# Kernel tuning notes

Hardware: AMD Instinct MI355X
Metric: run time of the kernel (lower is better)

## Reference

```python
import jax, jax.numpy as jnp
import numpy as np

H = 16  # n_heads


def setup_inputs() -> dict:
    key = jax.random.key(0)
    ks = jax.random.split(key, 11)
    B, S, D = 2, 2048, 1024
    def rn(k, shape, scale=1.0):
        return jax.random.normal(k, shape, dtype=jnp.float32) * scale
    w_scale = 1.0 / np.sqrt(D)
    return {
        "queries": rn(ks[0], (B, S, D)),
        "keys": rn(ks[1], (B, S, D)),
        "values": rn(ks[2], (B, S, D)),
        "Wq": rn(ks[3], (D, D), w_scale), "bq": rn(ks[4], (D,), 0.02),
        "Wk": rn(ks[5], (D, D), w_scale), "bk": rn(ks[6], (D,), 0.02),
        "Wv": rn(ks[7], (D, D), w_scale), "bv": rn(ks[8], (D,), 0.02),
        "Wo": rn(ks[9], (D, D), w_scale), "bo": rn(ks[10], (D,), 0.02),
    }


def _split_heads(x, h):
    # [B, S, D] -> [B, h, S, D/h]
    B, S, D = x.shape
    return x.reshape(B, S, h, D // h).transpose(0, 2, 1, 3)


def reference(queries, keys, values, Wq, bq, Wk, bk, Wv, bv, Wo, bo):
    B, S, D = queries.shape
    Q = _split_heads(queries @ Wq + bq, H)  # [B,h,S,dk]
    K = _split_heads(keys @ Wk + bk, H)
    V = _split_heads(values @ Wv + bv, H)
    # Faithful quirk: scale by sqrt(seq_len), not sqrt(d_k)
    factor = jnp.sqrt(jnp.asarray(S, dtype=Q.dtype))
    scores = jnp.einsum("bhqd,bhkd->bhqk", Q, K) / factor  # [B,h,S,S]
    weights = jax.nn.softmax(scores, axis=-1)
    attn = jnp.einsum("bhqk,bhkd->bhqd", weights, V)  # [B,h,S,dk]
    attn = attn.transpose(0, 2, 1, 3).reshape(B, S, D)  # [B,S,D]
    return attn @ Wo + bo
```

## Files before the change

### kernel.cpp

```cpp
#include <hip/hip_runtime.h>

typedef unsigned short ushort_t;
typedef unsigned int uint_t;
typedef __attribute__((ext_vector_type(8))) short short8;
typedef __attribute__((ext_vector_type(4))) float floatx4;

#define QSCALE 0.03187936f

__device__ __forceinline__ ushort_t f2bf(float f) {
    union { float f; uint_t u; } c; c.f = f;
    uint_t u = c.u;
    return (ushort_t)((u + 0x7fffu + ((u >> 16) & 1u)) >> 16);
}
__device__ __forceinline__ floatx4 mfma16x32(short8 a, short8 b, floatx4 c) {
    return __builtin_amdgcn_mfma_f32_16x16x32_bf16(a, b, c, 0, 0, 0);
}
__device__ __forceinline__ floatx4 zero4() { floatx4 z = {0.f, 0.f, 0.f, 0.f}; return z; }

__device__ __forceinline__ void gload16(const ushort_t* g, ushort_t* l) {
    __builtin_amdgcn_global_load_lds(
        (const __attribute__((address_space(1))) void*)g,
        (__attribute__((address_space(3))) void*)l, 16, 0, 0);
}

__global__ __launch_bounds__(256) void cvt_bf16(
    const float* __restrict__ s0, const float* __restrict__ s1,
    const float* __restrict__ s2, ushort_t* __restrict__ d0,
    ushort_t* __restrict__ d1, ushort_t* __restrict__ d2)
{
    const int which = blockIdx.x >> 11;
    const int blk = blockIdx.x & 2047;
    const float* src = (which == 0) ? s0 : (which == 1) ? s1 : s2;
    ushort_t* dst = (which == 0) ? d0 : (which == 1) ? d1 : d2;
    const int i = (blk * 256 + threadIdx.x) * 8;
    float4 f0 = *(const float4*)(src + i);
    float4 f1 = *(const float4*)(src + i + 4);
    __align__(16) ushort_t t[8];
    t[0] = f2bf(f0.x); t[1] = f2bf(f0.y); t[2] = f2bf(f0.z); t[3] = f2bf(f0.w);
    t[4] = f2bf(f1.x); t[5] = f2bf(f1.y); t[6] = f2bf(f1.z); t[7] = f2bf(f1.w);
    *(uint4*)(dst + i) = *(uint4*)t;
}

__global__ __launch_bounds__(256) void transpose_w(
    const float* __restrict__ W0, const float* __restrict__ W1,
    const float* __restrict__ W2, const float* __restrict__ W3,
    ushort_t* __restrict__ WT)
{
    __shared__ ushort_t tile[64][65];
    const float* W = (blockIdx.y == 0) ? W0 : (blockIdx.y == 1) ? W1
                   : (blockIdx.y == 2) ? W2 : W3;
    ushort_t* dst = WT + (size_t)blockIdx.y * (1024 * 1024);
    const int t = threadIdx.x;
    const int r = t >> 2, p = t & 3;
    const int j0 = (blockIdx.x & 15) << 6, k0 = (blockIdx.x >> 4) << 6;

    const float* src = W + (size_t)(k0 + r) * 1024 + j0 + p * 16;
    float4 f0 = *(const float4*)(src);
    float4 f1 = *(const float4*)(src + 4);
    float4 f2 = *(const float4*)(src + 8);
    float4 f3 = *(const float4*)(src + 12);
    ushort_t* tr = &tile[r][p * 16];
    tr[0] = f2bf(f0.x); tr[1] = f2bf(f0.y); tr[2]  = f2bf(f0.z); tr[3]  = f2bf(f0.w);
    tr[4] = f2bf(f1.x); tr[5] = f2bf(f1.y); tr[6]  = f2bf(f1.z); tr[7]  = f2bf(f1.w);
    tr[8] = f2bf(f2.x); tr[9] = f2bf(f2.y); tr[10] = f2bf(f2.z); tr[11] = f2bf(f2.w);
    tr[12] = f2bf(f3.x); tr[13] = f2bf(f3.y); tr[14] = f2bf(f3.z); tr[15] = f2bf(f3.w);
    __syncthreads();
    __align__(16) ushort_t buf[16];
#pragma unroll
    for (int i = 0; i < 16; ++i) buf[i] = tile[p * 16 + i][r];
    ushort_t* o = dst + (size_t)(j0 + r) * 1024 + k0 + p * 16;
    *(uint4*)(o)     = *(uint4*)(buf);
    *(uint4*)(o + 8) = *(uint4*)(buf + 8);
}

__global__ __launch_bounds__(256) void gemm_bt(
    const ushort_t* __restrict__ A0, const ushort_t* __restrict__ A1,
    const ushort_t* __restrict__ A2, const ushort_t* __restrict__ WT,
    const float* __restrict__ b0, const float* __restrict__ b1,
    const float* __restrict__ b2,
    ushort_t* __restrict__ Dq, ushort_t* __restrict__ Dk,
    ushort_t* __restrict__ Dv, int zbase)
{
    __shared__ __align__(16) ushort_t As[128 * 32];
    __shared__ __align__(16) ushort_t Bs[128 * 32];

    const int mode = blockIdx.z + zbase;
    const ushort_t* A = (mode == 0) ? A0 : (mode == 1) ? A1 : A2;
    const float* bias = (mode == 0) ? b0 : (mode == 1) ? b1 : b2;
    const ushort_t* Bt = WT + (size_t)mode * 1048576;

    const int tid = threadIdx.x;
    const int lane = tid & 63, wid = tid >> 6;
    const int quad = lane >> 4, l16 = lane & 15;
    const int wm = wid >> 1, wn = wid & 1;
    const int row0 = blockIdx.y << 7, col0 = blockIdx.x << 7;

    floatx4 acc[4][4];
#pragma unroll
    for (int i = 0; i < 4; ++i)
#pragma unroll
        for (int j = 0; j < 4; ++j) acc[i][j] = zero4();

    const int i0 = tid, i1 = 256 + tid;
    const int r0_ = i0 >> 2, c0_ = (i0 & 3) ^ (r0_ & 3);
    const int r1_ = i1 >> 2, c1_ = (i1 & 3) ^ (r1_ & 3);
    const ushort_t* gA0 = A  + (size_t)(row0 + r0_) * 1024 + c0_ * 8;
    const ushort_t* gA1 = A  + (size_t)(row0 + r1_) * 1024 + c1_ * 8;
    const ushort_t* gB0 = Bt + (size_t)(col0 + r0_) * 1024 + c0_ * 8;
    const ushort_t* gB1 = Bt + (size_t)(col0 + r1_) * 1024 + c1_ * 8;
    ushort_t* lA0 = As + i0 * 8;  ushort_t* lA1 = As + i1 * 8;
    ushort_t* lB0 = Bs + i0 * 8;  ushort_t* lB1 = Bs + i1 * 8;

    const int ra = wm * 64 + l16, rb = wn * 64 + l16;
    const int sa_off = (quad ^ (l16 & 3)) * 8;

    for (int k0 = 0; k0 < 1024; k0 += 32) {
        __syncthreads();
        gload16(gA0 + k0, lA0);
        gload16(gA1 + k0, lA1);
        gload16(gB0 + k0, lB0);
        gload16(gB1 + k0, lB1);
        __syncthreads();

        short8 af[4], bf[4];
#pragma unroll
        for (int i = 0; i < 4; ++i)
            af[i] = *(const short8*)(As + (ra + i * 16) * 32 + sa_off);
#pragma unroll
        for (int j = 0; j < 4; ++j)
            bf[j] = *(const short8*)(Bs + (rb + j * 16) * 32 + sa_off);
#pragma unroll
        for (int i = 0; i < 4; ++i)
#pragma unroll
            for (int j = 0; j < 4; ++j)
                acc[i][j] = mfma16x32(af[i], bf[j], acc[i][j]);
    }

    const float sc = (mode == 0) ? QSCALE : 1.f;
#pragma unroll
    for (int i = 0; i < 4; ++i) {
#pragma unroll
        for (int j = 0; j < 4; ++j) {
            const int c = col0 + wn * 64 + j * 16 + l16;
            const float bv = bias[c];
#pragma unroll
            for (int rr = 0; rr < 4; ++rr) {
                const int r = row0 + wm * 64 + i * 16 + quad * 4 + rr;
                const float v = (acc[i][j][rr] + bv) * sc;
                const int b = r >> 11, s = r & 2047, h = c >> 6, d = c & 63;
                if (mode <= 1) {
                    ushort_t* D = (mode == 0) ? Dq : Dk;
                    D[(((b * 16 + h) * 2048 + s) << 6) + d] = f2bf(v);
                } else {
                    Dv[(((b * 16 + h) * 64 + d) << 11) + s] = f2bf(v);
                }
            }
        }
    }
}

__global__ __launch_bounds__(256) void gemm64(
    const ushort_t* __restrict__ A, const ushort_t* __restrict__ Bt,
    const float* __restrict__ bias, float* __restrict__ Dout)
{
    __shared__ __align__(16) ushort_t As[64 * 32];
    __shared__ __align__(16) ushort_t Bs[128 * 32];
    const int tid = threadIdx.x;
    const int lane = tid & 63, wid = tid >> 6;
    const int quad = lane >> 4, l16 = lane & 15;
    const int wm = wid >> 1, wn = wid & 1;
    const int row0 = blockIdx.y << 6, col0 = blockIdx.x << 7;

    floatx4 acc[2][4];
#pragma unroll
    for (int i = 0; i < 2; ++i)
#pragma unroll
        for (int j = 0; j < 4; ++j) acc[i][j] = zero4();

    const int rA = tid >> 2, cA = (tid & 3) ^ (rA & 3);
    const ushort_t* gA = A + (size_t)(row0 + rA) * 1024 + cA * 8;
    ushort_t* lA = As + tid * 8;
    const int i0 = tid, i1 = 256 + tid;
    const int rB0 = i0 >> 2, cB0 = (i0 & 3) ^ (rB0 & 3);
    const int rB1 = i1 >> 2, cB1 = (i1 & 3) ^ (rB1 & 3);
    const ushort_t* gB0 = Bt + (size_t)(col0 + rB0) * 1024 + cB0 * 8;
    const ushort_t* gB1 = Bt + (size_t)(col0 + rB1) * 1024 + cB1 * 8;
    ushort_t* lB0 = Bs + i0 * 8;  ushort_t* lB1 = Bs + i1 * 8;

    const int sa_off = (quad ^ (l16 & 3)) * 8;

    for (int k0 = 0; k0 < 1024; k0 += 32) {
        __syncthreads();
        gload16(gA + k0, lA);
        gload16(gB0 + k0, lB0);
        gload16(gB1 + k0, lB1);
        __syncthreads();

        short8 af[2], bf[4];
#pragma unroll
        for (int i = 0; i < 2; ++i)
            af[i] = *(const short8*)(As + (wm * 32 + i * 16 + l16) * 32 + sa_off);
#pragma unroll
        for (int j = 0; j < 4; ++j)
            bf[j] = *(const short8*)(Bs + (wn * 64 + j * 16 + l16) * 32 + sa_off);
#pragma unroll
        for (int i = 0; i < 2; ++i)
#pragma unroll
            for (int j = 0; j < 4; ++j)
                acc[i][j] = mfma16x32(af[i], bf[j], acc[i][j]);
    }

#pragma unroll
    for (int i = 0; i < 2; ++i)
#pragma unroll
        for (int j = 0; j < 4; ++j) {
            const int c = col0 + wn * 64 + j * 16 + l16;
            const float bv = bias[c];
#pragma unroll
            for (int rr = 0; rr < 4; ++rr) {
                const int r = row0 + wm * 32 + i * 16 + quad * 4 + rr;
                Dout[(size_t)r * 1024 + c] = acc[i][j][rr] + bv;
            }
        }
}

__global__ __launch_bounds__(256, 2) void attn64q(
    const ushort_t* __restrict__ Q, const ushort_t* __restrict__ K,
    const ushort_t* __restrict__ Vt, ushort_t* __restrict__ Out)
{
    __shared__ __align__(16) ushort_t Ks[2][64 * 64];
    __shared__ __align__(16) ushort_t Vs[2][64 * 64];

    const int tid = threadIdx.x;
    const int lane = tid & 63, wid = tid >> 6;
    const int quad = lane >> 4, l16 = lane & 15;
    const int blk = blockIdx.x;
    const int bh = blk & 31;
    const int q0 = (blk >> 5) << 7;

    const ushort_t* Qh = Q + (size_t)bh * (2048 * 64);
    const ushort_t* Kh = K + (size_t)bh * (2048 * 64);
    const ushort_t* Vh = Vt + (size_t)bh * (64 * 2048);

    short8 qf0[2], qf1[2];
#pragma unroll
    for (int u = 0; u < 2; ++u) {
        const int qr = q0 + wid * 32 + u * 16 + l16;
        qf0[u] = *(const short8*)(Qh + (size_t)qr * 64 + quad * 8);
        qf1[u] = *(const short8*)(Qh + (size_t)qr * 64 + 32 + quad * 8);
    }

    floatx4 o_acc[2][4], lsum[2];
#pragma unroll
    for (int u = 0; u < 2; ++u) {
        lsum[u] = zero4();
#pragma unroll
        for (int d = 0; d < 4; ++d) o_acc[u][d] = zero4();
    }

    const int kr = tid >> 3, kc = (tid & 7) ^ (kr & 7);
    const ushort_t* gK0 = Kh + (size_t)kr * 64 + kc * 8;
    const ushort_t* gV0 = Vh + (size_t)kr * 2048 + kc * 8;
    ushort_t* lK0 = &Ks[0][0] + tid * 8;
    ushort_t* lV0 = &Vs[0][0] + tid * 8;

    const int l7 = l16 & 7;
    const int q2 = quad >> 1, q1 = (quad & 1) * 4;

    union { uint_t u4[4]; short8 s; } onep;
    onep.u4[0] = onep.u4[1] = onep.u4[2] = onep.u4[3] = 0x3f803f80u;
    const short8 ones = onep.s;

#define STAGE(pp, kto) do {                                            \
        gload16(gK0 + (size_t)(kto) * 64,         lK0 + (pp) * 4096);  \
        gload16(gK0 + (size_t)(kto) * 64 + 2048,  lK0 + (pp) * 4096 + 2048); \
        gload16(gV0 + (kto),                      lV0 + (pp) * 4096);  \
        gload16(gV0 + (kto) + 65536,              lV0 + (pp) * 4096 + 2048); \
    } while (0)

    STAGE(0, 0);
#pragma unroll 2
    for (int it = 0; it < 32; ++it) {
        const int p = it & 1;
        __syncthreads();
        if (it < 31) STAGE(p ^ 1, (it + 1) * 64);
        const ushort_t* ksp = &Ks[p][0];
        const ushort_t* vsp = &Vs[p][0];

        floatx4 sa[2][4];
#pragma unroll
        for (int g = 0; g < 4; ++g) {
            const int row = g * 16 + l16;
            const short8 kf0 = *(const short8*)(ksp + row * 64 + ((quad ^ l7) * 8));
            const short8 kf1 = *(const short8*)(ksp + row * 64 + (((quad + 4) ^ l7) * 8));
#pragma unroll
            for (int u = 0; u < 2; ++u) {
                floatx4 t0 = mfma16x32(kf0, qf0[u], zero4());
                sa[u][g] = mfma16x32(kf1, qf1[u], t0);
            }
        }

#pragma unroll
        for (int G = 0; G < 2; ++G) {
            short8 pf[2];
#pragma unroll
            for (int u = 0; u < 2; ++u) {
                uint_t ub[8];
#pragma unroll
                for (int t = 0; t < 8; ++t) {
                    const int g = G * 2 + (t >> 2), r = t & 3;
                    const float e = __builtin_amdgcn_exp2f(fminf(sa[u][g][r], 80.f));
                    ub[t] = __float_as_uint(e) & 0xffff0000u;
                }
                union { uint_t u4[4]; short8 s; } pc;
                pc.u4[0] = (ub[0] >> 16) | ub[1];
                pc.u4[1] = (ub[2] >> 16) | ub[3];
                pc.u4[2] = (ub[4] >> 16) | ub[5];
                pc.u4[3] = (ub[6] >> 16) | ub[7];
                pf[u] = pc.s;
                lsum[u] = mfma16x32(pf[u], ones, lsum[u]);
            }
            const int ch0 = ((4 * G + q2) ^ l7) * 8;
            const int ch1 = ((4 * G + 2 + q2) ^ l7) * 8;
#pragma unroll
            for (int db = 0; db < 4; ++db) {
                const int vbase = (db * 16 + l16) * 64 + q1;
                const uint2 v0 = *(const uint2*)(vsp + vbase + ch0);
                const uint2 v1 = *(const uint2*)(vsp + vbase + ch1);
                union { uint_t u4[4]; short8 s; } vc;
                vc.u4[0] = v0.x; vc.u4[1] = v0.y; vc.u4[2] = v1.x; vc.u4[3] = v1.y;
                o_acc[0][db] = mfma16x32(pf[0], vc.s, o_acc[0][db]);
                o_acc[1][db] = mfma16x32(pf[1], vc.s, o_acc[1][db]);
            }
        }
    }
#undef STAGE

    const int b = bh >> 4, hh = bh & 15;
#pragma unroll
    for (int u = 0; u < 2; ++u) {
        const int s0 = q0 + wid * 32 + u * 16 + quad * 4;
#pragma unroll
        for (int r = 0; r < 4; ++r) {
            const float inv = 1.f / lsum[u][r];
#pragma unroll
            for (int db = 0; db < 4; ++db) {
                const float v = o_acc[u][db][r] * inv;
                Out[(size_t)(b * 2048 + s0 + r) * 1024 + hh * 64 + db * 16 + l16] = f2bf(v);
            }
        }
    }
}

extern "C" void kernel_launch(void* const* d_in, const int* in_sizes, int n_in,
                              void* d_out, int out_size, void* d_ws, size_t ws_size,
                              hipStream_t stream) {
    const float* queries = (const float*)d_in[0];
    const float* keys    = (const float*)d_in[1];
    const float* values  = (const float*)d_in[2];
    const float* Wq = (const float*)d_in[3];
    const float* bq = (const float*)d_in[4];
    const float* Wk = (const float*)d_in[5];
    const float* bk = (const float*)d_in[6];
    const float* Wv = (const float*)d_in[7];
    const float* bv = (const float*)d_in[8];
    const float* Wo = (const float*)d_in[9];
    const float* bo = (const float*)d_in[10];
    float* out = (float*)d_out;

    char* ws = (char*)d_ws;
    const size_t MB = 1024 * 1024;
    ushort_t* WT = (ushort_t*)(ws);
    const ushort_t* WoT = WT + 3 * 1048576;
    dim3 tb(256);

    transpose_w<<<dim3(256, 4), tb, 0, stream>>>(Wq, Wk, Wv, Wo, WT);

    if (ws_size >= 64 * MB) {
        ushort_t* Qb  = (ushort_t*)(ws + 8 * MB);
        ushort_t* Kb  = (ushort_t*)(ws + 16 * MB);
        ushort_t* Vb  = (ushort_t*)(ws + 24 * MB);
        ushort_t* Qp  = (ushort_t*)(ws + 32 * MB);
        ushort_t* Kp  = (ushort_t*)(ws + 40 * MB);
        ushort_t* Vtp = (ushort_t*)(ws + 48 * MB);
        ushort_t* An  = (ushort_t*)(ws + 56 * MB);
        cvt_bf16<<<dim3(6144), tb, 0, stream>>>(queries, keys, values, Qb, Kb, Vb);
        gemm_bt<<<dim3(8, 32, 3), tb, 0, stream>>>(Qb, Kb, Vb, WT,
            bq, bk, bv, Qp, Kp, Vtp, 0);
        attn64q<<<dim3(512), tb, 0, stream>>>(Qp, Kp, Vtp, An);
        gemm64<<<dim3(8, 64), tb, 0, stream>>>(An, WoT, bo, out);
    } else {
        ushort_t* buf1 = (ushort_t*)(ws + 8 * MB);
        ushort_t* buf2 = (ushort_t*)(ws + 16 * MB);
        ushort_t* Qp   = (ushort_t*)(ws + 24 * MB);
        ushort_t* Kp   = (ushort_t*)(ws + 32 * MB);
        cvt_bf16<<<dim3(4096), tb, 0, stream>>>(queries, keys, keys, buf1, buf2, buf2);
        gemm_bt<<<dim3(8, 32, 2), tb, 0, stream>>>(buf1, buf2, buf2, WT,
            bq, bk, bk, Qp, Kp, Kp, 0);
        cvt_bf16<<<dim3(2048), tb, 0, stream>>>(values, values, values, buf1, buf1, buf1);
        gemm_bt<<<dim3(8, 32, 1), tb, 0, stream>>>(buf1, buf1, buf1, WT,
            bv, bv, bv, buf2, buf2, buf2, 2);
        attn64q<<<dim3(512), tb, 0, stream>>>(Qp, Kp, buf2, buf1);
        gemm64<<<dim3(8, 64), tb, 0, stream>>>(buf1, WoT, bo, out);
    }
}
```

Before: 230.6 us.

## Stage 128-key tiles per barrier and pack bf16 probabilities with perm

```diff
diff --git a/kernel.cpp b/kernel.cpp
--- a/kernel.cpp
+++ b/kernel.cpp
@@ -228,8 +228,8 @@
     const ushort_t* __restrict__ Q, const ushort_t* __restrict__ K,
     const ushort_t* __restrict__ Vt, ushort_t* __restrict__ Out)
 {
-    __shared__ __align__(16) ushort_t Ks[2][64 * 64];
-    __shared__ __align__(16) ushort_t Vs[2][64 * 64];
+    __shared__ __align__(16) ushort_t Ks[2][2][64 * 64];
+    __shared__ __align__(16) ushort_t Vs[2][2][64 * 64];
 
     const int tid = threadIdx.x;
     const int lane = tid & 63, wid = tid >> 6;
@@ -261,8 +261,6 @@
     const int kr = tid >> 3, kc = (tid & 7) ^ (kr & 7);
     const ushort_t* gK0 = Kh + (size_t)kr * 64 + kc * 8;
     const ushort_t* gV0 = Vh + (size_t)kr * 2048 + kc * 8;
-    ushort_t* lK0 = &Ks[0][0] + tid * 8;
-    ushort_t* lV0 = &Vs[0][0] + tid * 8;
 
     const int l7 = l16 & 7;
     const int q2 = quad >> 1, q1 = (quad & 1) * 4;
@@ -271,66 +269,76 @@
     onep.u4[0] = onep.u4[1] = onep.u4[2] = onep.u4[3] = 0x3f803f80u;
     const short8 ones = onep.s;
 
-#define STAGE(pp, kto) do {                                            \
-        gload16(gK0 + (size_t)(kto) * 64,         lK0 + (pp) * 4096);  \
-        gload16(gK0 + (size_t)(kto) * 64 + 2048,  lK0 + (pp) * 4096 + 2048); \
-        gload16(gV0 + (kto),                      lV0 + (pp) * 4096);  \
-        gload16(gV0 + (kto) + 65536,              lV0 + (pp) * 4096 + 2048); \
+#define STAGE(pp, kto) do {                                                  \
+        _Pragma("unroll")                                                    \
+        for (int hf_ = 0; hf_ < 2; ++hf_) {                                  \
+            gload16(gK0 + (size_t)(kto) * 64 + hf_ * 4096,                   \
+                    &Ks[pp][hf_][tid * 8]);                                  \
+            gload16(gK0 + (size_t)(kto) * 64 + hf_ * 4096 + 2048,            \
+                    &Ks[pp][hf_][tid * 8 + 2048]);                           \
+            gload16(gV0 + (kto) + hf_ * 64,                                  \
+                    &Vs[pp][hf_][tid * 8]);                                  \
+            gload16(gV0 + (kto) + hf_ * 64 + 65536,                          \
+                    &Vs[pp][hf_][tid * 8 + 2048]);                           \
+        }                                                                    \
     } while (0)
 
     STAGE(0, 0);
-#pragma unroll 2
-    for (int it = 0; it < 32; ++it) {
+    for (int it = 0; it < 16; ++it) {
         const int p = it & 1;
         __syncthreads();
-        if (it < 31) STAGE(p ^ 1, (it + 1) * 64);
-        const ushort_t* ksp = &Ks[p][0];
-        const ushort_t* vsp = &Vs[p][0];
-
-        floatx4 sa[2][4];
-#pragma unroll
-        for (int g = 0; g < 4; ++g) {
-            const int row = g * 16 + l16;
-            const short8 kf0 = *(const short8*)(ksp + row * 64 + ((quad ^ l7) * 8));
-            const short8 kf1 = *(const short8*)(ksp + row * 64 + (((quad + 4) ^ l7) * 8));
-#pragma unroll
-            for (int u = 0; u < 2; ++u) {
-                floatx4 t0 = mfma16x32(kf0, qf0[u], zero4());
-                sa[u][g] = mfma16x32(kf1, qf1[u], t0);
+        if (it < 15) STAGE(p ^ 1, (it + 1) * 128);
+
+#pragma unroll
+        for (int hf = 0; hf < 2; ++hf) {
+            const ushort_t* ksp = &Ks[p][hf][0];
+            const ushort_t* vsp = &Vs[p][hf][0];
+
+            floatx4 sa[2][4];
+#pragma unroll
+            for (int g = 0; g < 4; ++g) {
+                const int row = g * 16 + l16;
+                const short8 kf0 = *(const short8*)(ksp + row * 64 + ((quad ^ l7) * 8));
+                const short8 kf1 = *(const short8*)(ksp + row * 64 + (((quad + 4) ^ l7) * 8));
+#pragma unroll
+                for (int u = 0; u < 2; ++u) {
+                    floatx4 t0 = mfma16x32(kf0, qf0[u], zero4());
+                    sa[u][g] = mfma16x32(kf1, qf1[u], t0);
+                }
             }
-        }
-
-#pragma unroll
-        for (int G = 0; G < 2; ++G) {
-            short8 pf[2];
-#pragma unroll
-            for (int u = 0; u < 2; ++u) {
-                uint_t ub[8];
-#pragma unroll
-                for (int t = 0; t < 8; ++t) {
-                    const int g = G * 2 + (t >> 2), r = t & 3;
-                    const float e = __builtin_amdgcn_exp2f(fminf(sa[u][g][r], 80.f));
-                    ub[t] = __float_as_uint(e) & 0xffff0000u;
+
+#pragma unroll
+            for (int G = 0; G < 2; ++G) {
+                short8 pf[2];
+#pragma unroll
+                for (int u = 0; u < 2; ++u) {
+                    uint_t ub[8];
+#pragma unroll
+                    for (int t = 0; t < 8; ++t) {
+                        const int g = G * 2 + (t >> 2), r = t & 3;
+                        const float e = __builtin_amdgcn_exp2f(fminf(sa[u][g][r], 80.f));
+                        ub[t] = __float_as_uint(e);
+                    }
+                    union { uint_t u4[4]; short8 s; } pc;
+                    pc.u4[0] = __builtin_amdgcn_perm(ub[1], ub[0], 0x07060302u);
+                    pc.u4[1] = __builtin_amdgcn_perm(ub[3], ub[2], 0x07060302u);
+                    pc.u4[2] = __builtin_amdgcn_perm(ub[5], ub[4], 0x07060302u);
+                    pc.u4[3] = __builtin_amdgcn_perm(ub[7], ub[6], 0x07060302u);
+                    pf[u] = pc.s;
+                    lsum[u] = mfma16x32(pf[u], ones, lsum[u]);
                 }
-                union { uint_t u4[4]; short8 s; } pc;
-                pc.u4[0] = (ub[0] >> 16) | ub[1];
-                pc.u4[1] = (ub[2] >> 16) | ub[3];
-                pc.u4[2] = (ub[4] >> 16) | ub[5];
-                pc.u4[3] = (ub[6] >> 16) | ub[7];
-                pf[u] = pc.s;
-                lsum[u] = mfma16x32(pf[u], ones, lsum[u]);
-            }
-            const int ch0 = ((4 * G + q2) ^ l7) * 8;
-            const int ch1 = ((4 * G + 2 + q2) ^ l7) * 8;
-#pragma unroll
-            for (int db = 0; db < 4; ++db) {
-                const int vbase = (db * 16 + l16) * 64 + q1;
-                const uint2 v0 = *(const uint2*)(vsp + vbase + ch0);
-                const uint2 v1 = *(const uint2*)(vsp + vbase + ch1);
-                union { uint_t u4[4]; short8 s; } vc;
-                vc.u4[0] = v0.x; vc.u4[1] = v0.y; vc.u4[2] = v1.x; vc.u4[3] = v1.y;
-                o_acc[0][db] = mfma16x32(pf[0], vc.s, o_acc[0][db]);
-                o_acc[1][db] = mfma16x32(pf[1], vc.s, o_acc[1][db]);
+                const int ch0 = ((4 * G + q2) ^ l7) * 8;
+                const int ch1 = ((4 * G + 2 + q2) ^ l7) * 8;
+#pragma unroll
+                for (int db = 0; db < 4; ++db) {
+                    const int vbase = (db * 16 + l16) * 64 + q1;
+                    const uint2 v0 = *(const uint2*)(vsp + vbase + ch0);
+                    const uint2 v1 = *(const uint2*)(vsp + vbase + ch1);
+                    union { uint_t u4[4]; short8 s; } vc;
+                    vc.u4[0] = v0.x; vc.u4[1] = v0.y; vc.u4[2] = v1.x; vc.u4[3] = v1.y;
+                    o_acc[0][db] = mfma16x32(pf[0], vc.s, o_acc[0][db]);
+                    o_acc[1][db] = mfma16x32(pf[1], vc.s, o_acc[1][db]);
+                }
             }
         }
     }
```

Measured after the change: 229.6 us. No clear change (-0.4%).
